# Kernel optimization log

Hardware: AMD Instinct MI355X
Metric: run time of the kernel (lower is better)

Reference implementation:

```python
import jax, jax.numpy as jnp
import numpy as np

NUM_LEVELS = 16
LEVEL_DIM = 2
BASE_RES = 16
LOG2_T = 19
TABLE_SIZE = 2 ** LOG2_T
SIZE = 1.0  # default `size` arg of call()

# 8 trilinear corner offsets, shape [8, 3]
OFFSETS = jnp.array([[0, 0, 0], [0, 0, 1], [0, 1, 0], [0, 1, 1],
                     [1, 0, 0], [1, 0, 1], [1, 1, 0], [1, 1, 1]], dtype=jnp.int32)
# Spatial hash primes (uint32 wraparound reproduces TF int64 low-19-bit result exactly)
PRIMES = jnp.array([1, 2654435761, 805459861], dtype=jnp.uint32)


def setup_inputs() -> dict:
    key = jax.random.key(0)
    k1, k2 = jax.random.split(key)
    N = 524288
    x = jax.random.uniform(k1, (N, 3), dtype=jnp.float32)  # in [0,1); call() re-normalizes
    # tf.random_uniform_initializer(minval=-1e-4, maxval=1e-4)
    tables = jax.random.uniform(k2, (NUM_LEVELS, TABLE_SIZE, LEVEL_DIM),
                                dtype=jnp.float32, minval=-1e-4, maxval=1e-4)
    return {"x": x, "tables": tables}


def _encode(x, tables):
    # x: [N, 3] float32, tables: [L, T, D]
    x = jnp.clip((x + SIZE) / (2 * SIZE), 0.0, 1.0 - 1e-6)
    res = (BASE_RES * (2 ** jnp.arange(NUM_LEVELS))).astype(jnp.float32)  # [L]
    scaled = x[None, :, :] * res[:, None, None]          # [L, N, 3]
    floor_f = jnp.floor(scaled)
    frac = scaled - floor_f                              # [L, N, 3]
    floor_i = floor_f.astype(jnp.int32)

    corner = floor_i[:, :, None, :] + OFFSETS[None, None]          # [L, N, 8, 3]
    c = corner.astype(jnp.uint32)
    levels_u = jnp.arange(NUM_LEVELS, dtype=jnp.uint32)[:, None, None]
    hashed = (c[..., 0] * PRIMES[0]) ^ (c[..., 1] * PRIMES[1]) \
             ^ (c[..., 2] * PRIMES[2]) ^ levels_u                  # [L, N, 8]
    idx = (hashed & jnp.uint32(TABLE_SIZE - 1)).astype(jnp.int32)  # mod 2^19

    emb = jax.vmap(lambda t, i: t[i])(tables, idx)                 # [L, N, 8, D]
    # trilinear weights: prod over xyz of frac (if offset==1) else 1-frac
    w = jnp.prod(jnp.where(OFFSETS[None, None] == 1,
                           frac[:, :, None, :], 1.0 - frac[:, :, None, :]),
                 axis=-1)                                          # [L, N, 8]
    out = jnp.sum(emb * w[..., None], axis=2)                      # [L, N, D]
    # concat levels along feature dim -> [N, L*D]
    return out.transpose(1, 0, 2).reshape(x.shape[0], NUM_LEVELS * LEVEL_DIM)


def reference(x, tables):
    return _encode(x, tables)
```

## Files before the change

kernel.cpp:

```cpp
#include <hip/hip_runtime.h>
#include <stdint.h>

#define NUM_LEVELS 16
#define LEVEL_DIM 2
#define BASE_RES 16
#define LOG2_T 19
#define TABLE_SIZE (1u << LOG2_T)
#define TABLE_MASK (TABLE_SIZE - 1u)

#define CPL 256
#define BLOCK 256

typedef float v2f __attribute__((ext_vector_type(2)));
typedef float v4f __attribute__((ext_vector_type(4)));

__device__ __forceinline__ v2f encode_point(
    const float* __restrict__ x, const float* __restrict__ tb,
    int n, float res, uint32_t lv)
{
    float px = __builtin_nontemporal_load(x + (size_t)n * 3 + 0);
    float py = __builtin_nontemporal_load(x + (size_t)n * 3 + 1);
    float pz = __builtin_nontemporal_load(x + (size_t)n * 3 + 2);

    px = fminf(fmaxf((px + 1.0f) * 0.5f, 0.0f), 1.0f - 1e-6f);
    py = fminf(fmaxf((py + 1.0f) * 0.5f, 0.0f), 1.0f - 1e-6f);
    pz = fminf(fmaxf((pz + 1.0f) * 0.5f, 0.0f), 1.0f - 1e-6f);

    float sx = px * res, sy = py * res, sz = pz * res;
    float fx = floorf(sx), fy = floorf(sy), fz = floorf(sz);
    float tx = sx - fx, ty = sy - fy, tz = sz - fz;
    uint32_t ix = (uint32_t)(int32_t)fx;
    uint32_t iy = (uint32_t)(int32_t)fy;
    uint32_t iz = (uint32_t)(int32_t)fz;

    uint32_t hx0 = ix;
    uint32_t hx1 = ix + 1u;
    uint32_t hy0 = iy * 2654435761u;
    uint32_t hy1 = (iy + 1u) * 2654435761u;
    uint32_t hz0 = iz * 805459861u;
    uint32_t hz1 = (iz + 1u) * 805459861u;

    uint32_t idx0 = ((hx0 ^ hy0 ^ hz0 ^ lv) & TABLE_MASK) * 2u;
    uint32_t idx1 = ((hx0 ^ hy0 ^ hz1 ^ lv) & TABLE_MASK) * 2u;
    uint32_t idx2 = ((hx0 ^ hy1 ^ hz0 ^ lv) & TABLE_MASK) * 2u;
    uint32_t idx3 = ((hx0 ^ hy1 ^ hz1 ^ lv) & TABLE_MASK) * 2u;
    uint32_t idx4 = ((hx1 ^ hy0 ^ hz0 ^ lv) & TABLE_MASK) * 2u;
    uint32_t idx5 = ((hx1 ^ hy0 ^ hz1 ^ lv) & TABLE_MASK) * 2u;
    uint32_t idx6 = ((hx1 ^ hy1 ^ hz0 ^ lv) & TABLE_MASK) * 2u;
    uint32_t idx7 = ((hx1 ^ hy1 ^ hz1 ^ lv) & TABLE_MASK) * 2u;

    v2f e0 = *(const v2f*)(tb + idx0);
    v2f e1 = *(const v2f*)(tb + idx1);
    v2f e2 = *(const v2f*)(tb + idx2);
    v2f e3 = *(const v2f*)(tb + idx3);
    v2f e4 = *(const v2f*)(tb + idx4);
    v2f e5 = *(const v2f*)(tb + idx5);
    v2f e6 = *(const v2f*)(tb + idx6);
    v2f e7 = *(const v2f*)(tb + idx7);

    float wx0 = 1.0f - tx, wx1 = tx;
    float wy0 = 1.0f - ty, wy1 = ty;
    float wz0 = 1.0f - tz, wz1 = tz;

    float w0 = wx0 * wy0 * wz0;
    float w1 = wx0 * wy0 * wz1;
    float w2 = wx0 * wy1 * wz0;
    float w3 = wx0 * wy1 * wz1;
    float w4 = wx1 * wy0 * wz0;
    float w5 = wx1 * wy0 * wz1;
    float w6 = wx1 * wy1 * wz0;
    float w7 = wx1 * wy1 * wz1;

    v2f acc;
    acc.x = e0.x * w0 + e1.x * w1 + e2.x * w2 + e3.x * w3
          + e4.x * w4 + e5.x * w5 + e6.x * w6 + e7.x * w7;
    acc.y = e0.y * w0 + e1.y * w1 + e2.y * w2 + e3.y * w3
          + e4.y * w4 + e5.y * w5 + e6.y * w6 + e7.y * w7;
    return acc;
}

__global__ __launch_bounds__(256, 8) void gather_level_kernel(
    const float* __restrict__ x,
    const float* __restrict__ tables,
    float* __restrict__ ws,
    int N)
{
    int g = blockIdx.x;
    int half  = g / (8 * CPL);
    int h     = g % (8 * CPL);
    int level = (h & 7) + 8 * half;
    int chunk = h >> 3;
    int P     = (N + CPL - 1) / CPL;
    int base  = chunk * P;

    const float* tb = tables + (size_t)level * TABLE_SIZE * LEVEL_DIM;
    v2f* wrow = (v2f*)ws + (size_t)level * N;
    float res = (float)(BASE_RES << level);
    uint32_t lv = (uint32_t)level;

    for (int i = threadIdx.x; i < P; i += 2 * BLOCK) {
        int n0 = base + i;
        int n1 = base + i + BLOCK;
        bool ok0 = (n0 < N);
        bool ok1 = (i + BLOCK < P) && (n1 < N);

        if (ok0 && ok1) {
            v2f a0 = encode_point(x, tb, n0, res, lv);
            v2f a1 = encode_point(x, tb, n1, res, lv);
            __builtin_nontemporal_store(a0, wrow + n0);
            __builtin_nontemporal_store(a1, wrow + n1);
        } else if (ok0) {
            v2f a0 = encode_point(x, tb, n0, res, lv);
            __builtin_nontemporal_store(a0, wrow + n0);
        }
    }
}

__global__ __launch_bounds__(256) void transpose_kernel(
    const float* __restrict__ ws, float* __restrict__ out, int N)
{
    int n = blockIdx.x * blockDim.x + threadIdx.x;
    if (n >= N) return;

    v2f v[NUM_LEVELS];
    #pragma unroll
    for (int l = 0; l < NUM_LEVELS; ++l)
        v[l] = __builtin_nontemporal_load((const v2f*)ws + (size_t)l * N + n);

    v4f* o = (v4f*)(out + (size_t)n * (NUM_LEVELS * LEVEL_DIM));
    #pragma unroll
    for (int i = 0; i < 8; ++i) {
        v4f t;
        t.x = v[2 * i].x;     t.y = v[2 * i].y;
        t.z = v[2 * i + 1].x; t.w = v[2 * i + 1].y;
        o[i] = t;
    }
}

__global__ __launch_bounds__(256) void hashenc_fallback(
    const float* __restrict__ x, const float* __restrict__ tables,
    float* __restrict__ out, int N)
{
    int n = blockIdx.x * blockDim.x + threadIdx.x;
    if (n >= N) return;
    float* op = out + (size_t)n * (NUM_LEVELS * LEVEL_DIM);
    #pragma unroll 4
    for (int l = 0; l < NUM_LEVELS; ++l) {
        const float* tb = tables + (size_t)l * TABLE_SIZE * LEVEL_DIM;
        v2f a = encode_point(x, tb, n, (float)(BASE_RES << l), (uint32_t)l);
        *(v2f*)(op + l * 2) = a;
    }
}

extern "C" void kernel_launch(void* const* d_in, const int* in_sizes, int n_in,
                              void* d_out, int out_size, void* d_ws, size_t ws_size,
                              hipStream_t stream) {
    const float* x      = (const float*)d_in[0];
    const float* tables = (const float*)d_in[1];
    float* out          = (float*)d_out;
    int N = in_sizes[0] / 3;

    size_t ws_needed = (size_t)NUM_LEVELS * N * LEVEL_DIM * sizeof(float);
    if (ws_size >= ws_needed) {
        float* ws = (float*)d_ws;
        gather_level_kernel<<<NUM_LEVELS * CPL, BLOCK, 0, stream>>>(x, tables, ws, N);
        transpose_kernel<<<(N + BLOCK - 1) / BLOCK, BLOCK, 0, stream>>>(ws, out, N);
    } else {
        hashenc_fallback<<<(N + BLOCK - 1) / BLOCK, BLOCK, 0, stream>>>(x, tables, out, N);
    }
}
```

Before: 433.8 us.

## Pair x-adjacent hash corners into single 16-byte gathers and widen transpose

```diff
diff --git a/kernel.cpp b/kernel.cpp
--- a/kernel.cpp
+++ b/kernel.cpp
@@ -7,20 +7,136 @@
 #define LOG2_T 19
 #define TABLE_SIZE (1u << LOG2_T)
 #define TABLE_MASK (TABLE_SIZE - 1u)
+#define PAIR_MASK (TABLE_MASK & ~1u)
 
 #define CPL 256
 #define BLOCK 256
 
 typedef float v2f __attribute__((ext_vector_type(2)));
 typedef float v4f __attribute__((ext_vector_type(4)));
+
+__global__ __launch_bounds__(256, 6) void gather_level_kernel(
+    const float* __restrict__ x,
+    const float* __restrict__ tables,
+    float* __restrict__ ws,
+    int N)
+{
+    int g = blockIdx.x;
+    int half  = g / (8 * CPL);
+    int h     = g % (8 * CPL);
+    int level = (h & 7) + 8 * half;
+    int chunk = h >> 3;
+    int P     = (N + CPL - 1) / CPL;
+    int base  = chunk * P;
+
+    const float* tb = tables + (size_t)level * TABLE_SIZE * LEVEL_DIM;
+    const v4f*   tp = (const v4f*)tb;
+    v2f* wrow = (v2f*)ws + (size_t)level * N;
+    float res = (float)(BASE_RES << level);
+    uint32_t lv = (uint32_t)level;
+
+    for (int i = threadIdx.x; i < P; i += BLOCK) {
+        int n = base + i;
+        if (n >= N) break;
+
+        float px = x[(size_t)n * 3 + 0];
+        float py = x[(size_t)n * 3 + 1];
+        float pz = x[(size_t)n * 3 + 2];
+
+        px = fminf(fmaxf((px + 1.0f) * 0.5f, 0.0f), 1.0f - 1e-6f);
+        py = fminf(fmaxf((py + 1.0f) * 0.5f, 0.0f), 1.0f - 1e-6f);
+        pz = fminf(fmaxf((pz + 1.0f) * 0.5f, 0.0f), 1.0f - 1e-6f);
+
+        float sx = px * res, sy = py * res, sz = pz * res;
+        float fx = floorf(sx), fy = floorf(sy), fz = floorf(sz);
+        float tx = sx - fx, ty = sy - fy, tz = sz - fz;
+        uint32_t ix = (uint32_t)(int32_t)fx;
+        uint32_t iy = (uint32_t)(int32_t)fy;
+        uint32_t iz = (uint32_t)(int32_t)fz;
+
+        uint32_t hy0 = iy * 2654435761u;
+        uint32_t hy1 = (iy + 1u) * 2654435761u;
+        uint32_t hz0 = iz * 805459861u;
+        uint32_t hz1 = (iz + 1u) * 805459861u;
+        uint32_t m00 = hy0 ^ hz0 ^ lv;
+        uint32_t m01 = hy0 ^ hz1 ^ lv;
+        uint32_t m10 = hy1 ^ hz0 ^ lv;
+        uint32_t m11 = hy1 ^ hz1 ^ lv;
+
+        float wx1 = tx, wx0 = 1.0f - tx;
+        float wy1 = ty, wy0 = 1.0f - ty;
+        float wz1 = tz, wz0 = 1.0f - tz;
+        float w00 = wy0 * wz0, w01 = wy0 * wz1;
+        float w10 = wy1 * wz0, w11 = wy1 * wz1;
+
+        float ax, ay, bx, by;
+
+        if ((ix & 1u) == 0u) {
+            uint32_t h00 = ix ^ m00, h01 = ix ^ m01;
+            uint32_t h10 = ix ^ m10, h11 = ix ^ m11;
+            v4f p00 = tp[(h00 & PAIR_MASK) >> 1];
+            v4f p01 = tp[(h01 & PAIR_MASK) >> 1];
+            v4f p10 = tp[(h10 & PAIR_MASK) >> 1];
+            v4f p11 = tp[(h11 & PAIR_MASK) >> 1];
+            bool s00 = (h00 & 1u), s01 = (h01 & 1u);
+            bool s10 = (h10 & 1u), s11 = (h11 & 1u);
+            float a00x = s00 ? p00.z : p00.x, a00y = s00 ? p00.w : p00.y;
+            float b00x = s00 ? p00.x : p00.z, b00y = s00 ? p00.y : p00.w;
+            float a01x = s01 ? p01.z : p01.x, a01y = s01 ? p01.w : p01.y;
+            float b01x = s01 ? p01.x : p01.z, b01y = s01 ? p01.y : p01.w;
+            float a10x = s10 ? p10.z : p10.x, a10y = s10 ? p10.w : p10.y;
+            float b10x = s10 ? p10.x : p10.z, b10y = s10 ? p10.y : p10.w;
+            float a11x = s11 ? p11.z : p11.x, a11y = s11 ? p11.w : p11.y;
+            float b11x = s11 ? p11.x : p11.z, b11y = s11 ? p11.y : p11.w;
+            ax = a00x * w00 + a01x * w01 + a10x * w10 + a11x * w11;
+            ay = a00y * w00 + a01y * w01 + a10y * w10 + a11y * w11;
+            bx = b00x * w00 + b01x * w01 + b10x * w10 + b11x * w11;
+            by = b00y * w00 + b01y * w01 + b10y * w10 + b11y * w11;
+        } else {
+            uint32_t ja = ix, jb = ix + 1u;
+            v2f e00a = *(const v2f*)(tb + (size_t)(((ja ^ m00) & TABLE_MASK) * 2u));
+            v2f e01a = *(const v2f*)(tb + (size_t)(((ja ^ m01) & TABLE_MASK) * 2u));
+            v2f e10a = *(const v2f*)(tb + (size_t)(((ja ^ m10) & TABLE_MASK) * 2u));
+            v2f e11a = *(const v2f*)(tb + (size_t)(((ja ^ m11) & TABLE_MASK) * 2u));
+            v2f e00b = *(const v2f*)(tb + (size_t)(((jb ^ m00) & TABLE_MASK) * 2u));
+            v2f e01b = *(const v2f*)(tb + (size_t)(((jb ^ m01) & TABLE_MASK) * 2u));
+            v2f e10b = *(const v2f*)(tb + (size_t)(((jb ^ m10) & TABLE_MASK) * 2u));
+            v2f e11b = *(const v2f*)(tb + (size_t)(((jb ^ m11) & TABLE_MASK) * 2u));
+            ax = e00a.x * w00 + e01a.x * w01 + e10a.x * w10 + e11a.x * w11;
+            ay = e00a.y * w00 + e01a.y * w01 + e10a.y * w10 + e11a.y * w11;
+            bx = e00b.x * w00 + e01b.x * w01 + e10b.x * w10 + e11b.x * w11;
+            by = e00b.y * w00 + e01b.y * w01 + e10b.y * w10 + e11b.y * w11;
+        }
+
+        v2f acc;
+        acc.x = ax * wx0 + bx * wx1;
+        acc.y = ay * wx0 + by * wx1;
+        __builtin_nontemporal_store(acc, wrow + n);
+    }
+}
+
+__global__ __launch_bounds__(256) void transpose_kernel(
+    const float* __restrict__ ws, float* __restrict__ out, int N)
+{
+    int t = blockIdx.x * blockDim.x + threadIdx.x;
+    int p = t >> 3;
+    if (p >= N) return;
+    int c = t & 7;
+
+    v2f a = __builtin_nontemporal_load((const v2f*)ws + (size_t)(2 * c)     * N + p);
+    v2f b = __builtin_nontemporal_load((const v2f*)ws + (size_t)(2 * c + 1) * N + p);
+    v4f o;
+    o.x = a.x; o.y = a.y; o.z = b.x; o.w = b.y;
+    __builtin_nontemporal_store(o, (v4f*)out + (size_t)t);
+}
 
 __device__ __forceinline__ v2f encode_point(
     const float* __restrict__ x, const float* __restrict__ tb,
     int n, float res, uint32_t lv)
 {
-    float px = __builtin_nontemporal_load(x + (size_t)n * 3 + 0);
-    float py = __builtin_nontemporal_load(x + (size_t)n * 3 + 1);
-    float pz = __builtin_nontemporal_load(x + (size_t)n * 3 + 2);
+    float px = x[(size_t)n * 3 + 0];
+    float py = x[(size_t)n * 3 + 1];
+    float pz = x[(size_t)n * 3 + 2];
 
     px = fminf(fmaxf((px + 1.0f) * 0.5f, 0.0f), 1.0f - 1e-6f);
     py = fminf(fmaxf((py + 1.0f) * 0.5f, 0.0f), 1.0f - 1e-6f);
@@ -33,12 +149,9 @@
     uint32_t iy = (uint32_t)(int32_t)fy;
     uint32_t iz = (uint32_t)(int32_t)fz;
 
-    uint32_t hx0 = ix;
-    uint32_t hx1 = ix + 1u;
-    uint32_t hy0 = iy * 2654435761u;
-    uint32_t hy1 = (iy + 1u) * 2654435761u;
-    uint32_t hz0 = iz * 805459861u;
-    uint32_t hz1 = (iz + 1u) * 805459861u;
+    uint32_t hx0 = ix, hx1 = ix + 1u;
+    uint32_t hy0 = iy * 2654435761u, hy1 = (iy + 1u) * 2654435761u;
+    uint32_t hz0 = iz * 805459861u,  hz1 = (iz + 1u) * 805459861u;
 
     uint32_t idx0 = ((hx0 ^ hy0 ^ hz0 ^ lv) & TABLE_MASK) * 2u;
     uint32_t idx1 = ((hx0 ^ hy0 ^ hz1 ^ lv) & TABLE_MASK) * 2u;
@@ -77,64 +190,6 @@
     acc.y = e0.y * w0 + e1.y * w1 + e2.y * w2 + e3.y * w3
           + e4.y * w4 + e5.y * w5 + e6.y * w6 + e7.y * w7;
     return acc;
-}
-
-__global__ __launch_bounds__(256, 8) void gather_level_kernel(
-    const float* __restrict__ x,
-    const float* __restrict__ tables,
-    float* __restrict__ ws,
-    int N)
-{
-    int g = blockIdx.x;
-    int half  = g / (8 * CPL);
-    int h     = g % (8 * CPL);
-    int level = (h & 7) + 8 * half;
-    int chunk = h >> 3;
-    int P     = (N + CPL - 1) / CPL;
-    int base  = chunk * P;
-
-    const float* tb = tables + (size_t)level * TABLE_SIZE * LEVEL_DIM;
-    v2f* wrow = (v2f*)ws + (size_t)level * N;
-    float res = (float)(BASE_RES << level);
-    uint32_t lv = (uint32_t)level;
-
-    for (int i = threadIdx.x; i < P; i += 2 * BLOCK) {
-        int n0 = base + i;
-        int n1 = base + i + BLOCK;
-        bool ok0 = (n0 < N);
-        bool ok1 = (i + BLOCK < P) && (n1 < N);
-
-        if (ok0 && ok1) {
-            v2f a0 = encode_point(x, tb, n0, res, lv);
-            v2f a1 = encode_point(x, tb, n1, res, lv);
-            __builtin_nontemporal_store(a0, wrow + n0);
-            __builtin_nontemporal_store(a1, wrow + n1);
-        } else if (ok0) {
-            v2f a0 = encode_point(x, tb, n0, res, lv);
-            __builtin_nontemporal_store(a0, wrow + n0);
-        }
-    }
-}
-
-__global__ __launch_bounds__(256) void transpose_kernel(
-    const float* __restrict__ ws, float* __restrict__ out, int N)
-{
-    int n = blockIdx.x * blockDim.x + threadIdx.x;
-    if (n >= N) return;
-
-    v2f v[NUM_LEVELS];
-    #pragma unroll
-    for (int l = 0; l < NUM_LEVELS; ++l)
-        v[l] = __builtin_nontemporal_load((const v2f*)ws + (size_t)l * N + n);
-
-    v4f* o = (v4f*)(out + (size_t)n * (NUM_LEVELS * LEVEL_DIM));
-    #pragma unroll
-    for (int i = 0; i < 8; ++i) {
-        v4f t;
-        t.x = v[2 * i].x;     t.y = v[2 * i].y;
-        t.z = v[2 * i + 1].x; t.w = v[2 * i + 1].y;
-        o[i] = t;
-    }
 }
 
 __global__ __launch_bounds__(256) void hashenc_fallback(
@@ -164,7 +219,8 @@
     if (ws_size >= ws_needed) {
         float* ws = (float*)d_ws;
         gather_level_kernel<<<NUM_LEVELS * CPL, BLOCK, 0, stream>>>(x, tables, ws, N);
-        transpose_kernel<<<(N + BLOCK - 1) / BLOCK, BLOCK, 0, stream>>>(ws, out, N);
+        int tthreads = N * 8;
+        transpose_kernel<<<(tthreads + BLOCK - 1) / BLOCK, BLOCK, 0, stream>>>(ws, out, N);
     } else {
         hashenc_fallback<<<(N + BLOCK - 1) / BLOCK, BLOCK, 0, stream>>>(x, tables, out, N);
     }
```

Result: faster. 360.1 us (-17.0%).
